# Kernel optimization log

Measured on AMD Instinct MI355X. Metric: run time of the kernel, lower is better.

Reference implementation:

```python
import jax, jax.numpy as jnp
import numpy as np

REGION1 = REGION2 = 64
OVERLAP1 = OVERLAP2 = 0
MAX_M1 = MAX_M2 = 16


def dht1(x, axis):
    # 1D discrete Hartley transform along `axis` (real - imag of FFT)
    X = jnp.fft.fft(x, axis=axis)
    return X.real - X.imag


def dht2(x):
    # 2D DHT over last two axes
    X = jnp.fft.fft2(x, axes=(-2, -1))
    return X.real - X.imag


def flip_periodic2(x):
    # Faithful to torch code: flatten last two dims jointly, keep element 0, flip the rest
    s = x.shape
    n = s[-2] * s[-1]
    xf = x.reshape(s[:-2] + (n,))
    zf = jnp.concatenate([xf[..., :1], xf[..., 1:][..., ::-1]], axis=-1)
    return zf.reshape(s)


def hartley_conv2(x, y):
    # x: [b, i, h, w], y: [i, o, h, w] -> [b, o, h, w]; conv via Hartley theorem then idht
    X = dht2(x)
    Y = dht2(y)
    Xf = flip_periodic2(X)
    Yf = flip_periodic2(Y)
    Ye = 0.5 * (Y + Yf)
    Yo = 0.5 * (Y - Yf)
    Z = jnp.einsum('bihw,iohw->bohw', X, Ye) + jnp.einsum('bihw,iohw->bohw', Xf, Yo)
    n = x.shape[-2] * x.shape[-1]
    return dht2(Z) / n  # idht2 (DHT is involutory up to 1/n)


def spectral_conv2d(x, error_np, weights):
    B, Cin, S1, S2 = x.shape
    Cout = weights.shape[1]
    stride1 = REGION1 - OVERLAP1
    stride2 = REGION2 - OVERLAP2
    nr1 = (S1 - OVERLAP1) // stride1 + (1 if (S1 - OVERLAP1) % stride1 else 0)
    nr2 = (S2 - OVERLAP2) // stride2 + (1 if (S2 - OVERLAP2) % stride2 else 0)
    out = jnp.zeros((B, Cout, S1, S2), x.dtype)
    counts = np.zeros((S1, S2), np.float32)
    for i in range(nr1):
        for j in range(nr2):
            s1 = i * stride1; e1 = s1 + REGION1
            if e1 > S1:
                e1 = S1; s1 = max(e1 - REGION1, 0)
            s2 = j * stride2; e2 = s2 + REGION2
            if e2 > S2:
                e2 = S2; s2 = max(e2 - REGION2, 0)
            region_x = x[:, :, s1:e1, s2:e2]
            # adaptive per-sample mode counts from error signal (static, numpy)
            avg = error_np[:, s1:e1, s2:e2].mean(axis=(1, 2))
            mn, mx = avg.min(), avg.max()
            norm = (avg - mn) / (mx - mn) if (mx - mn) > 1e-8 else np.zeros_like(avg)
            nm1 = np.minimum((norm * (MAX_M1 - 1)).astype(np.int64) + 1, MAX_M1)
            nm2 = np.minimum((norm * (MAX_M2 - 1)).astype(np.int64) + 1, MAX_M2)
            # separable per-axis DHT of the region
            region_ht = dht1(dht1(region_x, -2), -1)
            out_ht = jnp.zeros((B, Cout, REGION1, REGION2), x.dtype)
            for b in range(B):
                n1 = int(nm1[b]); n2 = int(nm2[b])
                blk = hartley_conv2(region_ht[b:b + 1, :, :n1, :n2], weights[:, :, :n1, :n2])
                out_ht = out_ht.at[b, :, :n1, :n2].set(blk[0])
            # separable inverse per-axis DHT: dht1 along each axis / region area
            region_out = dht1(dht1(out_ht, -2), -1) / (REGION1 * REGION2)
            out = out.at[:, :, s1:e1, s2:e2].add(region_out)
            counts[s1:e1, s2:e2] += 1
    counts[counts == 0] = 1
    return out / jnp.asarray(counts, x.dtype)


def setup_inputs() -> dict:
    key = jax.random.key(0)
    k1, k2, k3 = jax.random.split(key, 3)
    B, Cin, Cout, S = 8, 32, 32, 256
    scale = 1.0 / (Cin * Cout)
    x = jax.random.normal(k1, (B, Cin, S, S), dtype=jnp.float32)
    error_signal = jax.random.uniform(k2, (B, S, S), dtype=jnp.float32)
    weights = scale * jax.random.uniform(k3, (Cin, Cout, MAX_M1, MAX_M2), dtype=jnp.float32)
    return {"x": x, "error_signal": error_signal, "weights": weights}


def reference(x, error_signal, weights):
    error_np = np.asarray(error_signal)
    return spectral_conv2d(x, error_np, weights)
```

## Files before the change

### kernel.cpp

```cpp
#include <hip/hip_runtime.h>
#include <math.h>

#define NB 8
#define CIN 32
#define COUT 32
#define SS 256
#define REG 64
#define NMAX 16

#define AVG_OFF   0
#define C64_OFF   4096
#define CN_OFF    4352
#define Y_OFF     8192
#define XE_OFF    (8u << 20)
#define XO_OFF    (12u << 20)
#define Z_OFF     (16u << 20)

__device__ __forceinline__ int region_n(const float* __restrict__ avg, int r, int b) {
    float mn = avg[r * 8], mx = mn;
    for (int bb = 1; bb < NB; ++bb) {
        float v = avg[r * 8 + bb];
        mn = fminf(mn, v);
        mx = fmaxf(mx, v);
    }
    float d = mx - mn;
    bool ok = ((double)d > 1e-8);
    float norm = ok ? (avg[r * 8 + b] - mn) / d : 0.0f;
    float tt = norm * 15.0f;
    int nv = (int)tt + 1;
    return nv > NMAX ? NMAX : nv;
}

__global__ void k_avg(const float* __restrict__ err, float* __restrict__ avg,
                      float* __restrict__ cyc64, float* __restrict__ cycN) {
    int t = threadIdx.x;
    if (blockIdx.x == 16) {
        if (blockIdx.y != 0) return;
        if (t < 64) {
            double a = (2.0 * M_PI / 64.0) * (double)t;
            cyc64[t] = (float)(cos(a) + sin(a));
        } else if (t < 64 + 136) {
            int e = t - 64;
            int n = 1;
            while (n * (n + 1) / 2 <= e) ++n;
            int j = e - n * (n - 1) / 2;
            double a = (2.0 * M_PI / (double)n) * (double)j;
            cycN[e] = (float)(cos(a) + sin(a));
        }
        return;
    }
    int r = blockIdx.x, b = blockIdx.y;
    int ri = r >> 2, rj = r & 3;
    const float* base = err + ((size_t)b * SS + ri * REG) * SS + rj * REG;
    double s = 0.0;
    for (int it = 0; it < 16; ++it) {
        int u = it * 4 + (t >> 6);
        int v = t & 63;
        s += (double)base[(size_t)u * SS + v];
    }
    __shared__ double sm[256];
    sm[t] = s;
    __syncthreads();
    for (int w = 128; w > 0; w >>= 1) {
        if (t < w) sm[t] += sm[t + w];
        __syncthreads();
    }
    if (t == 0) avg[r * 8 + b] = (float)(sm[0] / 4096.0);
}

__global__ void k_fwd(const float* __restrict__ x, const float* __restrict__ avg,
                      const float* __restrict__ cyc64, const float* __restrict__ cycN,
                      float* __restrict__ Xe, float* __restrict__ Xo) {
    int i = blockIdx.x, r = blockIdx.y, b = blockIdx.z;
    int n = region_n(avg, r, b);
    int nn = n * n;
    int ri = r >> 2, rj = r & 3;
    int t = threadIdx.x;

    __shared__ __align__(16) float R[64 * 64];
    __shared__ __align__(16) float M1[16 * 68];
    __shared__ float H[256];
    __shared__ float T1[256];
    __shared__ float T2[256];
    __shared__ float cyc64L[64];
    __shared__ float cnL[16];

    if (t < 64) cyc64L[t] = cyc64[t];
    if (t < n)  cnL[t] = cycN[(n * (n - 1)) / 2 + t];

    const float* base = x + (((size_t)(b * CIN + i)) * SS + ri * REG) * SS + rj * REG;
    float4* R4 = (float4*)R;
    {
        int u0 = t >> 4, c4 = t & 15;
        for (int it = 0; it < 4; ++it) {
            int u = it * 16 + u0;
            R4[u * 16 + c4] = *(const float4*)(base + (size_t)u * SS + c4 * 4);
        }
    }
    __syncthreads();

    {
        int uq = t >> 6, ps = (t >> 4) & 3, vg = t & 15;
        int p0 = ps, p1 = ps + 4, p2 = ps + 8, p3 = ps + 12;
        int i0 = (p0 * (uq << 4)) & 63;
        int i1 = (p1 * (uq << 4)) & 63;
        int i2 = (p2 * (uq << 4)) & 63;
        int i3 = (p3 * (uq << 4)) & 63;
        float4 a0 = {0.f,0.f,0.f,0.f}, a1 = a0, a2 = a0, a3 = a0;
        int ubase = (uq << 4) * 16 + vg;
        for (int uu = 0; uu < 16; ++uu) {
            float4 rv = R4[ubase + uu * 16];
            if (p0 < n) { float c = cyc64L[i0];
                a0.x += c*rv.x; a0.y += c*rv.y; a0.z += c*rv.z; a0.w += c*rv.w; }
            if (p1 < n) { float c = cyc64L[i1];
                a1.x += c*rv.x; a1.y += c*rv.y; a1.z += c*rv.z; a1.w += c*rv.w; }
            if (p2 < n) { float c = cyc64L[i2];
                a2.x += c*rv.x; a2.y += c*rv.y; a2.z += c*rv.z; a2.w += c*rv.w; }
            if (p3 < n) { float c = cyc64L[i3];
                a3.x += c*rv.x; a3.y += c*rv.y; a3.z += c*rv.z; a3.w += c*rv.w; }
            i0 = (i0 + p0) & 63; i1 = (i1 + p1) & 63;
            i2 = (i2 + p2) & 63; i3 = (i3 + p3) & 63;
        }
        __syncthreads();
        float4* P4 = R4;
        int pb = (uq << 8) + vg;
        if (p0 < n) P4[pb + p0 * 16] = a0;
        if (p1 < n) P4[pb + p1 * 16] = a1;
        if (p2 < n) P4[pb + p2 * 16] = a2;
        if (p3 < n) P4[pb + p3 * 16] = a3;
        __syncthreads();
        int pr = t >> 4, vr = t & 15;
        if (pr < n) {
            float4 q0 = P4[pr * 16 + vr];
            float4 q1 = P4[256 + pr * 16 + vr];
            float4 q2 = P4[512 + pr * 16 + vr];
            float4 q3 = P4[768 + pr * 16 + vr];
            float4 s;
            s.x = (q0.x + q1.x) + (q2.x + q3.x);
            s.y = (q0.y + q1.y) + (q2.y + q3.y);
            s.z = (q0.z + q1.z) + (q2.z + q3.z);
            s.w = (q0.w + q1.w) + (q2.w + q3.w);
            *(float4*)&M1[pr * 68 + vr * 4] = s;
        }
    }
    __syncthreads();

    int p = 0, q = 0;
    if (t < nn) { p = t / n; q = t - p * n; }

    if (t < nn) {
        float acc = 0.f;
        int idx = 0;
        for (int v = 0; v < 64; ++v) {
            acc += M1[p * 68 + v] * cyc64L[idx];
            idx = (idx + q) & 63;
        }
        H[t] = acc;
    }
    __syncthreads();

    if (t < nn) {
        float acc = 0.f;
        int idx = 0;
        for (int v = 0; v < n; ++v) {
            acc += H[p * n + v] * cnL[idx];
            idx += q; if (idx >= n) idx -= n;
        }
        T1[p * n + q] = acc;
    }
    __syncthreads();
    if (t < nn) {
        float acc = 0.f;
        int idx = 0;
        for (int u = 0; u < n; ++u) {
            acc += T1[u * n + q] * cnL[idx];
            idx += p; if (idx >= n) idx -= n;
        }
        T2[t] = acc;
    }
    __syncthreads();
    if (t < nn) {
        int pf = (p == 0) ? 0 : n - p;
        int qf = (q == 0) ? 0 : n - q;
        H[t] = 0.5f * (T2[p * n + q] + T2[pf * n + q] + T2[p * n + qf] - T2[pf * n + qf]);
    }
    __syncthreads();

    if (t < nn) {
        int fk = (t == 0) ? 0 : nn - t;
        float a = H[t], c = H[fk];
        size_t o = (((size_t)(b * 16 + r)) * CIN + i) * 256 + t;
        Xe[o] = 0.5f * (a + c);
        Xo[o] = 0.5f * (a - c);
    }
}

__global__ void k_wt(const float* __restrict__ wts, const float* __restrict__ cycN,
                     float* __restrict__ Y) {
    int io = blockIdx.x;
    int t = threadIdx.x;
    __shared__ float Wt[256];
    __shared__ float T1[256];
    __shared__ float T2[256];
    __shared__ float cnL[16];
    Wt[t] = wts[(size_t)io * 256 + t];
    for (int n = 1; n <= NMAX; ++n) {
        int nn = n * n;
        __syncthreads();
        if (t < n) cnL[t] = cycN[(n * (n - 1)) / 2 + t];
        __syncthreads();
        int p = 0, q = 0;
        if (t < nn) { p = t / n; q = t - p * n; }
        if (t < nn) {
            float acc = 0.f;
            int idx = 0;
            for (int v = 0; v < n; ++v) {
                acc += Wt[p * 16 + v] * cnL[idx];
                idx += q; if (idx >= n) idx -= n;
            }
            T1[p * n + q] = acc;
        }
        __syncthreads();
        if (t < nn) {
            float acc = 0.f;
            int idx = 0;
            for (int u = 0; u < n; ++u) {
                acc += T1[u * n + q] * cnL[idx];
                idx += p; if (idx >= n) idx -= n;
            }
            T2[t] = acc;
        }
        __syncthreads();
        if (t < nn) {
            int pf = (p == 0) ? 0 : n - p;
            int qf = (q == 0) ? 0 : n - q;
            float v = 0.5f * (T2[p * n + q] + T2[pf * n + q] + T2[p * n + qf] - T2[pf * n + qf]);
            int m = n - 1;
            int ps2 = m * (m + 1) * (2 * m + 1) / 6;
            Y[(size_t)1024 * ps2 + (size_t)io * nn + t] = v;
        }
    }
}

__global__ void k_z(const float* __restrict__ Xe, const float* __restrict__ Xo,
                    const float* __restrict__ Y, const float* __restrict__ avg,
                    float* __restrict__ Z) {
    int br = blockIdx.y;
    int og = blockIdx.x * 4;
    int b = br >> 4, r = br & 15;
    int n = region_n(avg, r, b);
    int nn = n * n;
    int t = threadIdx.x;
    if (t >= nn) return;
    int m = n - 1;
    int ps2 = m * (m + 1) * (2 * m + 1) / 6;
    const float* Yb = Y + (size_t)1024 * ps2;
    int fk = (t == 0) ? 0 : nn - t;
    float acc[4] = {0.f, 0.f, 0.f, 0.f};
    size_t xbase = (size_t)br * CIN * 256;
#pragma unroll 2
    for (int i = 0; i < CIN; ++i) {
        float xe = Xe[xbase + i * 256 + t];
        float xo = Xo[xbase + i * 256 + t];
        const float* yi = Yb + (size_t)(i * COUT + og) * nn;
#pragma unroll
        for (int oo = 0; oo < 4; ++oo) {
            acc[oo] += xe * yi[oo * nn + t] + xo * yi[oo * nn + fk];
        }
    }
    size_t zbase = (size_t)br * COUT * 256;
#pragma unroll
    for (int oo = 0; oo < 4; ++oo) Z[zbase + (og + oo) * 256 + t] = acc[oo];
}

__global__ void k_out(const float* __restrict__ Z, const float* __restrict__ avg,
                      const float* __restrict__ cyc64, const float* __restrict__ cycN,
                      float* __restrict__ out) {
    int o = blockIdx.x, r = blockIdx.y, b = blockIdx.z;
    int n = region_n(avg, r, b);
    int nn = n * n;
    int t = threadIdx.x;
    int br = b * 16 + r;

    __shared__ float Zs[256];
    __shared__ float T1[256];
    __shared__ float T2[256];
    __shared__ float Bk[256];
    __shared__ __align__(16) float E1[16 * 64];
    __shared__ float cyc64L[64];
    __shared__ float cnL[16];

    if (t < 64) cyc64L[t] = cyc64[t];
    if (t < n)  cnL[t] = cycN[(n * (n - 1)) / 2 + t];
    if (t < nn) Zs[t] = Z[((size_t)br * COUT + o) * 256 + t];
    __syncthreads();

    int p = 0, q = 0;
    if (t < nn) { p = t / n; q = t - p * n; }

    if (t < nn) {
        float acc = 0.f;
        int idx = 0;
        for (int v = 0; v < n; ++v) {
            acc += Zs[p * n + v] * cnL[idx];
            idx += q; if (idx >= n) idx -= n;
        }
        T1[p * n + q] = acc;
    }
    __syncthreads();
    if (t < nn) {
        float acc = 0.f;
        int idx = 0;
        for (int u = 0; u < n; ++u) {
            acc += T1[u * n + q] * cnL[idx];
            idx += p; if (idx >= n) idx -= n;
        }
        T2[t] = acc;
    }
    __syncthreads();
    if (t < nn) {
        int pf = (p == 0) ? 0 : n - p;
        int qf = (q == 0) ? 0 : n - q;
        Bk[t] = 0.5f * (T2[p * n + q] + T2[pf * n + q] + T2[p * n + qf] - T2[pf * n + qf])
                / (float)nn;
    }
    __syncthreads();

    for (int mm = t; mm < n * 64; mm += 256) {
        int pp = mm >> 6, v = mm & 63;
        float acc = 0.f;
        int idx = 0;
        for (int qq = 0; qq < n; ++qq) {
            acc += Bk[pp * n + qq] * cyc64L[idx];
            idx = (idx + v) & 63;
        }
        E1[pp * 64 + v] = acc;
    }
    __syncthreads();

    int ri = r >> 2, rj = r & 3;
    float* ob = out + (((size_t)(b * COUT + o)) * SS + ri * REG) * SS + rj * REG;
    const float4* E14 = (const float4*)E1;
    const float inv = 1.0f / 4096.0f;
    int u0 = t >> 4, vg = t & 15;
    int uA = u0, uB = 16 + u0, uC = 32 + u0, uD = 48 + u0;
    int iA = 0, iB = 0, iC = 0, iD = 0;
    float4 aA = {0.f,0.f,0.f,0.f}, aB = aA, aC = aA, aD = aA;
    for (int pp = 0; pp < n; ++pp) {
        float4 e = E14[pp * 16 + vg];
        float cA = cyc64L[iA]; iA = (iA + uA) & 63;
        float cB = cyc64L[iB]; iB = (iB + uB) & 63;
        float cC = cyc64L[iC]; iC = (iC + uC) & 63;
        float cD = cyc64L[iD]; iD = (iD + uD) & 63;
        aA.x += cA*e.x; aA.y += cA*e.y; aA.z += cA*e.z; aA.w += cA*e.w;
        aB.x += cB*e.x; aB.y += cB*e.y; aB.z += cB*e.z; aB.w += cB*e.w;
        aC.x += cC*e.x; aC.y += cC*e.y; aC.z += cC*e.z; aC.w += cC*e.w;
        aD.x += cD*e.x; aD.y += cD*e.y; aD.z += cD*e.z; aD.w += cD*e.w;
    }
    aA.x *= inv; aA.y *= inv; aA.z *= inv; aA.w *= inv;
    aB.x *= inv; aB.y *= inv; aB.z *= inv; aB.w *= inv;
    aC.x *= inv; aC.y *= inv; aC.z *= inv; aC.w *= inv;
    aD.x *= inv; aD.y *= inv; aD.z *= inv; aD.w *= inv;
    *(float4*)(ob + (size_t)uA * SS + vg * 4) = aA;
    *(float4*)(ob + (size_t)uB * SS + vg * 4) = aB;
    *(float4*)(ob + (size_t)uC * SS + vg * 4) = aC;
    *(float4*)(ob + (size_t)uD * SS + vg * 4) = aD;
}

extern "C" void kernel_launch(void* const* d_in, const int* in_sizes, int n_in,
                              void* d_out, int out_size, void* d_ws, size_t ws_size,
                              hipStream_t stream) {
    const float* x   = (const float*)d_in[0];
    const float* err = (const float*)d_in[1];
    const float* wts = (const float*)d_in[2];
    float* out = (float*)d_out;
    char* ws = (char*)d_ws;

    float* avg   = (float*)(ws + AVG_OFF);
    float* cyc64 = (float*)(ws + C64_OFF);
    float* cycN  = (float*)(ws + CN_OFF);
    float* Y     = (float*)(ws + Y_OFF);
    float* Xe    = (float*)(ws + XE_OFF);
    float* Xo    = (float*)(ws + XO_OFF);
    float* Z     = (float*)(ws + Z_OFF);

    k_avg<<<dim3(17, NB), 256, 0, stream>>>(err, avg, cyc64, cycN);
    k_wt<<<dim3(CIN * COUT), 256, 0, stream>>>(wts, cycN, Y);
    k_fwd<<<dim3(CIN, 16, NB), 256, 0, stream>>>(x, avg, cyc64, cycN, Xe, Xo);
    k_z<<<dim3(8, 128), 256, 0, stream>>>(Xe, Xo, Y, avg, Z);
    k_out<<<dim3(COUT, 16, NB), 256, 0, stream>>>(Z, avg, cyc64, cycN, out);
}
```

Measured before the change: 182.6 us.

## Fuse avg and weight-transform kernels, fuse Z contraction with inverse transform

Merges the error-average and weight Hartley transform kernels into one prep launch that also writes a flipped copy of Y. The Z contraction and the output inverse transform are fused into one kernel, so the Z round-trip through global memory and one launch are removed. Twiddle products for the final stage are precomputed into a shared table. The fused output kernel runs only 1024 blocks, each handling 4 output channels in sequence, so the final stage has less parallelism than the previous 4096-block launch.

New measurement: 181.2 us. About the same (-0.8%).

```diff
diff --git a/kernel.cpp b/kernel.cpp
--- a/kernel.cpp
+++ b/kernel.cpp
@@ -12,9 +12,9 @@
 #define C64_OFF   4096
 #define CN_OFF    4352
 #define Y_OFF     8192
-#define XE_OFF    (8u << 20)
-#define XO_OFF    (12u << 20)
-#define Z_OFF     (16u << 20)
+#define YF_OFF    (8u << 20)
+#define XE_OFF    (16u << 20)
+#define XO_OFF    (20u << 20)
 
 __device__ __forceinline__ int region_n(const float* __restrict__ avg, int r, int b) {
     float mn = avg[r * 8], mx = mn;
@@ -31,11 +31,35 @@
     return nv > NMAX ? NMAX : nv;
 }
 
-__global__ void k_avg(const float* __restrict__ err, float* __restrict__ avg,
-                      float* __restrict__ cyc64, float* __restrict__ cycN) {
+__global__ void k_prep(const float* __restrict__ err, const float* __restrict__ wts,
+                       float* __restrict__ avg, float* __restrict__ cyc64,
+                       float* __restrict__ cycN, float* __restrict__ Y,
+                       float* __restrict__ Yf) {
+    int bx = blockIdx.x;
     int t = threadIdx.x;
-    if (blockIdx.x == 16) {
-        if (blockIdx.y != 0) return;
+
+    if (bx < 128) {
+        int r = bx & 15, b = bx >> 4;
+        int ri = r >> 2, rj = r & 3;
+        const float* base = err + ((size_t)b * SS + ri * REG) * SS + rj * REG;
+        double s = 0.0;
+        for (int it = 0; it < 16; ++it) {
+            int u = it * 4 + (t >> 6);
+            int v = t & 63;
+            s += (double)base[(size_t)u * SS + v];
+        }
+        __shared__ double sm[256];
+        sm[t] = s;
+        __syncthreads();
+        for (int w = 128; w > 0; w >>= 1) {
+            if (t < w) sm[t] += sm[t + w];
+            __syncthreads();
+        }
+        if (t == 0) avg[r * 8 + b] = (float)(sm[0] / 4096.0);
+        return;
+    }
+
+    if (bx == 128) {
         if (t < 64) {
             double a = (2.0 * M_PI / 64.0) * (double)t;
             cyc64[t] = (float)(cos(a) + sin(a));
@@ -49,23 +73,61 @@
         }
         return;
     }
-    int r = blockIdx.x, b = blockIdx.y;
-    int ri = r >> 2, rj = r & 3;
-    const float* base = err + ((size_t)b * SS + ri * REG) * SS + rj * REG;
-    double s = 0.0;
-    for (int it = 0; it < 16; ++it) {
-        int u = it * 4 + (t >> 6);
-        int v = t & 63;
-        s += (double)base[(size_t)u * SS + v];
-    }
-    __shared__ double sm[256];
-    sm[t] = s;
-    __syncthreads();
-    for (int w = 128; w > 0; w >>= 1) {
-        if (t < w) sm[t] += sm[t + w];
-        __syncthreads();
-    }
-    if (t == 0) avg[r * 8 + b] = (float)(sm[0] / 4096.0);
+
+    int io = bx - 129;
+    __shared__ float Wt[256];
+    __shared__ float T1[256];
+    __shared__ float T2[256];
+    __shared__ float cnAll[136];
+    if (t < 136) {
+        int e = t;
+        int n = 1;
+        while (n * (n + 1) / 2 <= e) ++n;
+        int j = e - n * (n - 1) / 2;
+        double a = (2.0 * M_PI / (double)n) * (double)j;
+        cnAll[e] = (float)(cos(a) + sin(a));
+    }
+    Wt[t] = wts[(size_t)io * 256 + t];
+    __syncthreads();
+
+    for (int n = 1; n <= NMAX; ++n) {
+        int nn = n * n;
+        const float* cnL = &cnAll[(n * (n - 1)) / 2];
+        int p = 0, q = 0;
+        if (t < nn) { p = t / n; q = t - p * n; }
+        if (t < nn) {
+            float acc = 0.f;
+            int idx = 0;
+            for (int v = 0; v < n; ++v) {
+                acc += Wt[p * 16 + v] * cnL[idx];
+                idx += q; if (idx >= n) idx -= n;
+            }
+            T1[p * n + q] = acc;
+        }
+        __syncthreads();
+        if (t < nn) {
+            float acc = 0.f;
+            int idx = 0;
+            for (int u = 0; u < n; ++u) {
+                acc += T1[u * n + q] * cnL[idx];
+                idx += p; if (idx >= n) idx -= n;
+            }
+            T2[t] = acc;
+        }
+        __syncthreads();
+        if (t < nn) {
+            int pf = (p == 0) ? 0 : n - p;
+            int qf = (q == 0) ? 0 : n - q;
+            float v = 0.5f * (T2[p * n + q] + T2[pf * n + q] + T2[p * n + qf] - T2[pf * n + qf]);
+            int m = n - 1;
+            int ps2 = m * (m + 1) * (2 * m + 1) / 6;
+            size_t basei = (size_t)1024 * ps2 + (size_t)io * nn;
+            Y[basei + t] = v;
+            int fk = (t == 0) ? 0 : nn - t;
+            Yf[basei + fk] = v;
+        }
+        __syncthreads();
+    }
 }
 
 __global__ void k_fwd(const float* __restrict__ x, const float* __restrict__ avg,
@@ -195,27 +257,75 @@
     }
 }
 
-__global__ void k_wt(const float* __restrict__ wts, const float* __restrict__ cycN,
-                     float* __restrict__ Y) {
-    int io = blockIdx.x;
+__global__ void k_zout(const float* __restrict__ Xe, const float* __restrict__ Xo,
+                       const float* __restrict__ Y, const float* __restrict__ Yf,
+                       const float* __restrict__ avg, const float* __restrict__ cyc64,
+                       const float* __restrict__ cycN, float* __restrict__ out) {
+    int og = blockIdx.x * 4;
+    int br = blockIdx.y;
+    int b = br >> 4, r = br & 15;
+    int n = region_n(avg, r, b);
+    int nn = n * n;
     int t = threadIdx.x;
-    __shared__ float Wt[256];
+
+    __shared__ float zbuf[4][256];
     __shared__ float T1[256];
     __shared__ float T2[256];
+    __shared__ float Bk[256];
+    __shared__ __align__(16) float E1[16 * 64];
+    __shared__ __align__(16) float CTo[16 * 16 * 4];
+    __shared__ float cyc64L[64];
     __shared__ float cnL[16];
-    Wt[t] = wts[(size_t)io * 256 + t];
-    for (int n = 1; n <= NMAX; ++n) {
-        int nn = n * n;
-        __syncthreads();
-        if (t < n) cnL[t] = cycN[(n * (n - 1)) / 2 + t];
-        __syncthreads();
-        int p = 0, q = 0;
-        if (t < nn) { p = t / n; q = t - p * n; }
+
+    if (t < 64) cyc64L[t] = cyc64[t];
+    if (t < n)  cnL[t] = cycN[(n * (n - 1)) / 2 + t];
+    __syncthreads();
+
+    {
+        int pp = t >> 4, u0 = t & 15;
+        float4 c;
+        c.x = cyc64L[(pp * u0) & 63];
+        c.y = cyc64L[(pp * (u0 + 16)) & 63];
+        c.z = cyc64L[(pp * (u0 + 32)) & 63];
+        c.w = cyc64L[(pp * (u0 + 48)) & 63];
+        *(float4*)&CTo[t * 4] = c;
+    }
+
+    if (t < nn) {
+        int m = n - 1;
+        int ps2 = m * (m + 1) * (2 * m + 1) / 6;
+        const float* Yb  = Y  + (size_t)1024 * ps2;
+        const float* Yfb = Yf + (size_t)1024 * ps2;
+        float a0 = 0.f, a1 = 0.f, a2 = 0.f, a3 = 0.f;
+        size_t xbase = (size_t)br * CIN * 256;
+        for (int i = 0; i < CIN; ++i) {
+            float xe = Xe[xbase + i * 256 + t];
+            float xo = Xo[xbase + i * 256 + t];
+            const float* yp  = Yb  + (size_t)(i * COUT + og) * nn + t;
+            const float* yfp = Yfb + (size_t)(i * COUT + og) * nn + t;
+            a0 += xe * yp[0]      + xo * yfp[0];
+            a1 += xe * yp[nn]     + xo * yfp[nn];
+            a2 += xe * yp[2 * nn] + xo * yfp[2 * nn];
+            a3 += xe * yp[3 * nn] + xo * yfp[3 * nn];
+        }
+        zbuf[0][t] = a0; zbuf[1][t] = a1; zbuf[2][t] = a2; zbuf[3][t] = a3;
+    }
+
+    int p = 0, q = 0;
+    if (t < nn) { p = t / n; q = t - p * n; }
+    int ri = r >> 2, rj = r & 3;
+    int u0 = t >> 4, vg = t & 15;
+    const float4* E14 = (const float4*)E1;
+    const float4* CT4 = (const float4*)CTo;
+    const float inv = 1.0f / 4096.0f;
+
+    for (int oo = 0; oo < 4; ++oo) {
+        __syncthreads();
         if (t < nn) {
             float acc = 0.f;
             int idx = 0;
             for (int v = 0; v < n; ++v) {
-                acc += Wt[p * 16 + v] * cnL[idx];
+                acc += zbuf[oo][p * n + v] * cnL[idx];
                 idx += q; if (idx >= n) idx -= n;
             }
             T1[p * n + q] = acc;
@@ -234,137 +344,40 @@
         if (t < nn) {
             int pf = (p == 0) ? 0 : n - p;
             int qf = (q == 0) ? 0 : n - q;
-            float v = 0.5f * (T2[p * n + q] + T2[pf * n + q] + T2[p * n + qf] - T2[pf * n + qf]);
-            int m = n - 1;
-            int ps2 = m * (m + 1) * (2 * m + 1) / 6;
-            Y[(size_t)1024 * ps2 + (size_t)io * nn + t] = v;
-        }
-    }
-}
-
-__global__ void k_z(const float* __restrict__ Xe, const float* __restrict__ Xo,
-                    const float* __restrict__ Y, const float* __restrict__ avg,
-                    float* __restrict__ Z) {
-    int br = blockIdx.y;
-    int og = blockIdx.x * 4;
-    int b = br >> 4, r = br & 15;
-    int n = region_n(avg, r, b);
-    int nn = n * n;
-    int t = threadIdx.x;
-    if (t >= nn) return;
-    int m = n - 1;
-    int ps2 = m * (m + 1) * (2 * m + 1) / 6;
-    const float* Yb = Y + (size_t)1024 * ps2;
-    int fk = (t == 0) ? 0 : nn - t;
-    float acc[4] = {0.f, 0.f, 0.f, 0.f};
-    size_t xbase = (size_t)br * CIN * 256;
-#pragma unroll 2
-    for (int i = 0; i < CIN; ++i) {
-        float xe = Xe[xbase + i * 256 + t];
-        float xo = Xo[xbase + i * 256 + t];
-        const float* yi = Yb + (size_t)(i * COUT + og) * nn;
-#pragma unroll
-        for (int oo = 0; oo < 4; ++oo) {
-            acc[oo] += xe * yi[oo * nn + t] + xo * yi[oo * nn + fk];
-        }
-    }
-    size_t zbase = (size_t)br * COUT * 256;
-#pragma unroll
-    for (int oo = 0; oo < 4; ++oo) Z[zbase + (og + oo) * 256 + t] = acc[oo];
-}
-
-__global__ void k_out(const float* __restrict__ Z, const float* __restrict__ avg,
-                      const float* __restrict__ cyc64, const float* __restrict__ cycN,
-                      float* __restrict__ out) {
-    int o = blockIdx.x, r = blockIdx.y, b = blockIdx.z;
-    int n = region_n(avg, r, b);
-    int nn = n * n;
-    int t = threadIdx.x;
-    int br = b * 16 + r;
-
-    __shared__ float Zs[256];
-    __shared__ float T1[256];
-    __shared__ float T2[256];
-    __shared__ float Bk[256];
-    __shared__ __align__(16) float E1[16 * 64];
-    __shared__ float cyc64L[64];
-    __shared__ float cnL[16];
-
-    if (t < 64) cyc64L[t] = cyc64[t];
-    if (t < n)  cnL[t] = cycN[(n * (n - 1)) / 2 + t];
-    if (t < nn) Zs[t] = Z[((size_t)br * COUT + o) * 256 + t];
-    __syncthreads();
-
-    int p = 0, q = 0;
-    if (t < nn) { p = t / n; q = t - p * n; }
-
-    if (t < nn) {
-        float acc = 0.f;
-        int idx = 0;
-        for (int v = 0; v < n; ++v) {
-            acc += Zs[p * n + v] * cnL[idx];
-            idx += q; if (idx >= n) idx -= n;
-        }
-        T1[p * n + q] = acc;
-    }
-    __syncthreads();
-    if (t < nn) {
-        float acc = 0.f;
-        int idx = 0;
-        for (int u = 0; u < n; ++u) {
-            acc += T1[u * n + q] * cnL[idx];
-            idx += p; if (idx >= n) idx -= n;
-        }
-        T2[t] = acc;
-    }
-    __syncthreads();
-    if (t < nn) {
-        int pf = (p == 0) ? 0 : n - p;
-        int qf = (q == 0) ? 0 : n - q;
-        Bk[t] = 0.5f * (T2[p * n + q] + T2[pf * n + q] + T2[p * n + qf] - T2[pf * n + qf])
-                / (float)nn;
-    }
-    __syncthreads();
-
-    for (int mm = t; mm < n * 64; mm += 256) {
-        int pp = mm >> 6, v = mm & 63;
-        float acc = 0.f;
-        int idx = 0;
-        for (int qq = 0; qq < n; ++qq) {
-            acc += Bk[pp * n + qq] * cyc64L[idx];
-            idx = (idx + v) & 63;
-        }
-        E1[pp * 64 + v] = acc;
-    }
-    __syncthreads();
-
-    int ri = r >> 2, rj = r & 3;
-    float* ob = out + (((size_t)(b * COUT + o)) * SS + ri * REG) * SS + rj * REG;
-    const float4* E14 = (const float4*)E1;
-    const float inv = 1.0f / 4096.0f;
-    int u0 = t >> 4, vg = t & 15;
-    int uA = u0, uB = 16 + u0, uC = 32 + u0, uD = 48 + u0;
-    int iA = 0, iB = 0, iC = 0, iD = 0;
-    float4 aA = {0.f,0.f,0.f,0.f}, aB = aA, aC = aA, aD = aA;
-    for (int pp = 0; pp < n; ++pp) {
-        float4 e = E14[pp * 16 + vg];
-        float cA = cyc64L[iA]; iA = (iA + uA) & 63;
-        float cB = cyc64L[iB]; iB = (iB + uB) & 63;
-        float cC = cyc64L[iC]; iC = (iC + uC) & 63;
-        float cD = cyc64L[iD]; iD = (iD + uD) & 63;
-        aA.x += cA*e.x; aA.y += cA*e.y; aA.z += cA*e.z; aA.w += cA*e.w;
-        aB.x += cB*e.x; aB.y += cB*e.y; aB.z += cB*e.z; aB.w += cB*e.w;
-        aC.x += cC*e.x; aC.y += cC*e.y; aC.z += cC*e.z; aC.w += cC*e.w;
-        aD.x += cD*e.x; aD.y += cD*e.y; aD.z += cD*e.z; aD.w += cD*e.w;
-    }
-    aA.x *= inv; aA.y *= inv; aA.z *= inv; aA.w *= inv;
-    aB.x *= inv; aB.y *= inv; aB.z *= inv; aB.w *= inv;
-    aC.x *= inv; aC.y *= inv; aC.z *= inv; aC.w *= inv;
-    aD.x *= inv; aD.y *= inv; aD.z *= inv; aD.w *= inv;
-    *(float4*)(ob + (size_t)uA * SS + vg * 4) = aA;
-    *(float4*)(ob + (size_t)uB * SS + vg * 4) = aB;
-    *(float4*)(ob + (size_t)uC * SS + vg * 4) = aC;
-    *(float4*)(ob + (size_t)uD * SS + vg * 4) = aD;
+            Bk[t] = 0.5f * (T2[p * n + q] + T2[pf * n + q] + T2[p * n + qf] - T2[pf * n + qf])
+                    / (float)nn;
+        }
+        __syncthreads();
+        for (int mm = t; mm < n * 64; mm += 256) {
+            int pp = mm >> 6, v = mm & 63;
+            float acc = 0.f;
+            int idx = 0;
+            for (int qq = 0; qq < n; ++qq) {
+                acc += Bk[pp * n + qq] * cyc64L[idx];
+                idx = (idx + v) & 63;
+            }
+            E1[pp * 64 + v] = acc;
+        }
+        __syncthreads();
+        float* ob = out + (((size_t)(b * COUT + og + oo)) * SS + ri * REG) * SS + rj * REG;
+        float4 aA = {0.f,0.f,0.f,0.f}, aB = aA, aC = aA, aD = aA;
+        for (int pp = 0; pp < n; ++pp) {
+            float4 e = E14[pp * 16 + vg];
+            float4 c = CT4[pp * 16 + u0];
+            aA.x += c.x*e.x; aA.y += c.x*e.y; aA.z += c.x*e.z; aA.w += c.x*e.w;
+            aB.x += c.y*e.x; aB.y += c.y*e.y; aB.z += c.y*e.z; aB.w += c.y*e.w;
+            aC.x += c.z*e.x; aC.y += c.z*e.y; aC.z += c.z*e.z; aC.w += c.z*e.w;
+            aD.x += c.w*e.x; aD.y += c.w*e.y; aD.z += c.w*e.z; aD.w += c.w*e.w;
+        }
+        aA.x *= inv; aA.y *= inv; aA.z *= inv; aA.w *= inv;
+        aB.x *= inv; aB.y *= inv; aB.z *= inv; aB.w *= inv;
+        aC.x *= inv; aC.y *= inv; aC.z *= inv; aC.w *= inv;
+        aD.x *= inv; aD.y *= inv; aD.z *= inv; aD.w *= inv;
+        *(float4*)(ob + (size_t)(u0)      * SS + vg * 4) = aA;
+        *(float4*)(ob + (size_t)(16 + u0) * SS + vg * 4) = aB;
+        *(float4*)(ob + (size_t)(32 + u0) * SS + vg * 4) = aC;
+        *(float4*)(ob + (size_t)(48 + u0) * SS + vg * 4) = aD;
+    }
 }
 
 extern "C" void kernel_launch(void* const* d_in, const int* in_sizes, int n_in,
@@ -380,13 +393,11 @@
     float* cyc64 = (float*)(ws + C64_OFF);
     float* cycN  = (float*)(ws + CN_OFF);
     float* Y     = (float*)(ws + Y_OFF);
+    float* Yf    = (float*)(ws + YF_OFF);
     float* Xe    = (float*)(ws + XE_OFF);
     float* Xo    = (float*)(ws + XO_OFF);
-    float* Z     = (float*)(ws + Z_OFF);
-
-    k_avg<<<dim3(17, NB), 256, 0, stream>>>(err, avg, cyc64, cycN);
-    k_wt<<<dim3(CIN * COUT), 256, 0, stream>>>(wts, cycN, Y);
+
+    k_prep<<<dim3(128 + 1 + CIN * COUT), 256, 0, stream>>>(err, wts, avg, cyc64, cycN, Y, Yf);
     k_fwd<<<dim3(CIN, 16, NB), 256, 0, stream>>>(x, avg, cyc64, cycN, Xe, Xo);
-    k_z<<<dim3(8, 128), 256, 0, stream>>>(Xe, Xo, Y, avg, Z);
-    k_out<<<dim3(COUT, 16, NB), 256, 0, stream>>>(Z, avg, cyc64, cycN, out);
+    k_zout<<<dim3(8, 128), 256, 0, stream>>>(Xe, Xo, Y, Yf, avg, cyc64, cycN, out);
 }
```
